# Kernel optimization log

Measured on AMD Instinct MI355X. Metric: run time of the kernel, lower is better.

## Reference

```python
import jax, jax.numpy as jnp
import numpy as np

L = 2        # num GRU layers
H = 1024     # hidden_size
V = 50257    # output_size (vocab)


def setup_inputs() -> dict:
    key = jax.random.key(0)
    ks = jax.random.split(key, 10)
    s = 1.0 / np.sqrt(H)
    return {
        "input_tok": jax.random.randint(ks[0], (1,), 0, V, dtype=jnp.int64),
        "hidden": jax.random.normal(ks[1], (L, 1, H), dtype=jnp.float32),
        "emb": jax.random.normal(ks[2], (V, H), dtype=jnp.float32),
        "W_ih": jax.random.uniform(ks[3], (L, 3 * H, H), jnp.float32, -s, s),
        "W_hh": jax.random.uniform(ks[4], (L, 3 * H, H), jnp.float32, -s, s),
        "b_ih": jax.random.uniform(ks[5], (L, 3 * H), jnp.float32, -s, s),
        "b_hh": jax.random.uniform(ks[6], (L, 3 * H), jnp.float32, -s, s),
        "W_out": jax.random.uniform(ks[7], (V, H), jnp.float32, -s, s),
        "b_out": jax.random.uniform(ks[8], (V,), jnp.float32, -s, s),
    }


def _gru_step(x, hidden, W_ih, W_hh, b_ih, b_hh):
    # x: [1, H] single-timestep input; hidden: [L, 1, H]
    # PyTorch GRU gate order: r, z, n
    new_h = []
    for l in range(L):
        h = hidden[l]                                   # [1, H]
        gi = x @ W_ih[l].T + b_ih[l]                    # [1, 3H]
        gh = h @ W_hh[l].T + b_hh[l]                    # [1, 3H]
        gi_r, gi_z, gi_n = gi[:, :H], gi[:, H:2 * H], gi[:, 2 * H:]
        gh_r, gh_z, gh_n = gh[:, :H], gh[:, H:2 * H], gh[:, 2 * H:]
        r = jax.nn.sigmoid(gi_r + gh_r)
        z = jax.nn.sigmoid(gi_z + gh_z)
        n = jnp.tanh(gi_n + r * gh_n)
        h_new = (1.0 - z) * n + z * h                   # [1, H]
        new_h.append(h_new)
        x = h_new                                       # feed next layer (eval: no dropout)
    return x, jnp.stack(new_h, axis=0)                  # [1,H], [L,1,H]


def reference(input_tok, hidden, emb, W_ih, W_hh, b_ih, b_hh, W_out, b_out):
    # embedding lookup + view(1,1,-1) -> relu
    x = jax.nn.relu(emb[input_tok[0]]).reshape(1, H)     # [1, H] (seq dim of 1 folded)
    out, hidden_new = _gru_step(x, hidden, W_ih, W_hh, b_ih, b_hh)
    logits = out @ W_out.T + b_out                       # [1, V]
    logprobs = jax.nn.log_softmax(logits, axis=1)        # LogSoftmax(dim=1)
    return logprobs, hidden_new
```

## Files before the change

### kernel.cpp

```cpp
#include <hip/hip_runtime.h>
#include <cstdint>
#include <math.h>

#define H 1024
#define V 50257
#define PBLK 2048

__device__ __forceinline__ float dot4(float4 a, float4 b) {
    return a.x * b.x + a.y * b.y + a.z * b.z + a.w * b.w;
}

__global__ __launch_bounds__(256) void gru_layer(
    const float* __restrict__ emb, const int* __restrict__ tok, int use_emb,
    const float* __restrict__ xvec,
    const float* __restrict__ hprev,
    const float* __restrict__ Wih, const float* __restrict__ Whh,
    const float* __restrict__ bih, const float* __restrict__ bhh,
    float* __restrict__ hnew_ws, float* __restrict__ hnew_out)
{
    const int i = blockIdx.x;
    const int t = threadIdx.x;

    const float* xb = use_emb ? (emb + (size_t)tok[0] * (size_t)H) : xvec;
    float4 xv = *(const float4*)(xb + 4 * t);
    if (use_emb) {
        xv.x = fmaxf(xv.x, 0.f); xv.y = fmaxf(xv.y, 0.f);
        xv.z = fmaxf(xv.z, 0.f); xv.w = fmaxf(xv.w, 0.f);
    }

    float s[6];
    {
        const float* r0 = Wih + (size_t)i * H;
        const float* r1 = Wih + (size_t)(H + i) * H;
        const float* r2 = Wih + (size_t)(2 * H + i) * H;
        const float* r3 = Whh + (size_t)i * H;
        const float* r4 = Whh + (size_t)(H + i) * H;
        const float* r5 = Whh + (size_t)(2 * H + i) * H;
        s[0] = dot4(*(const float4*)(r0 + 4 * t), xv);
        s[1] = dot4(*(const float4*)(r1 + 4 * t), xv);
        s[2] = dot4(*(const float4*)(r2 + 4 * t), xv);
        float4 hv = *(const float4*)(hprev + 4 * t);
        s[3] = dot4(*(const float4*)(r3 + 4 * t), hv);
        s[4] = dot4(*(const float4*)(r4 + 4 * t), hv);
        s[5] = dot4(*(const float4*)(r5 + 4 * t), hv);
    }

    #pragma unroll
    for (int m = 1; m < 64; m <<= 1) {
        #pragma unroll
        for (int k = 0; k < 6; ++k) s[k] += __shfl_xor(s[k], m);
    }
    __shared__ float red[4][6];
    const int wv = t >> 6, ln = t & 63;
    if (ln == 0) {
        #pragma unroll
        for (int k = 0; k < 6; ++k) red[wv][k] = s[k];
    }
    __syncthreads();
    if (t == 0) {
        float g[6];
        #pragma unroll
        for (int k = 0; k < 6; ++k)
            g[k] = red[0][k] + red[1][k] + red[2][k] + red[3][k];
        float gir = g[0] + bih[i], giz = g[1] + bih[H + i], gin = g[2] + bih[2 * H + i];
        float ghr = g[3] + bhh[i], ghz = g[4] + bhh[H + i], ghn = g[5] + bhh[2 * H + i];
        float r = 1.f / (1.f + expf(-(gir + ghr)));
        float z = 1.f / (1.f + expf(-(giz + ghz)));
        float n = tanhf(gin + r * ghn);
        float hp = hprev[i];
        float hn = (1.f - z) * n + z * hp;
        hnew_ws[i] = hn;
        hnew_out[i] = hn;
    }
}

__global__ __launch_bounds__(256) void proj_kernel(
    const float* __restrict__ h, const float* __restrict__ Wout,
    const float* __restrict__ bout, float* __restrict__ logits,
    float* __restrict__ pmax, float* __restrict__ psum)
{
    const int t = threadIdx.x;
    const int wv = t >> 6, ln = t & 63;
    const int gw = blockIdx.x * 4 + wv;
    const int nw = PBLK * 4;

    float4 hr[4];
    #pragma unroll
    for (int j = 0; j < 4; ++j) hr[j] = *(const float4*)(h + 4 * (ln + 64 * j));

    float wmax = -INFINITY, wsum = 0.f;
    for (int v = gw; v < V; v += nw) {
        const float* wrow = Wout + (size_t)v * H;
        float s = 0.f;
        #pragma unroll
        for (int j = 0; j < 4; ++j)
            s += dot4(*(const float4*)(wrow + 4 * (ln + 64 * j)), hr[j]);
        #pragma unroll
        for (int m = 1; m < 64; m <<= 1) s += __shfl_xor(s, m);
        s += bout[v];
        if (ln == 0) logits[v] = s;
        float nm = fmaxf(wmax, s);
        wsum = wsum * expf(wmax - nm) + expf(s - nm);
        wmax = nm;
    }
    __shared__ float smax[4], ssum[4];
    if (ln == 0) { smax[wv] = wmax; ssum[wv] = wsum; }
    __syncthreads();
    if (t == 0) {
        float m = fmaxf(fmaxf(smax[0], smax[1]), fmaxf(smax[2], smax[3]));
        float su = 0.f;
        #pragma unroll
        for (int w = 0; w < 4; ++w) su += ssum[w] * expf(smax[w] - m);
        pmax[blockIdx.x] = m;
        psum[blockIdx.x] = su;
    }
}

__global__ __launch_bounds__(256) void finalize_kernel(
    float* __restrict__ logits,
    const float* __restrict__ pmax, const float* __restrict__ psum)
{
    const int t = threadIdx.x;
    float m = -INFINITY, su = 0.f;
    for (int i = t; i < PBLK; i += 256) {
        float om = pmax[i], os = psum[i];
        float nm = fmaxf(m, om);
        su = su * expf(m - nm) + os * expf(om - nm);
        m = nm;
    }
    #pragma unroll
    for (int k = 1; k < 64; k <<= 1) {
        float om = __shfl_xor(m, k), os = __shfl_xor(su, k);
        float nm = fmaxf(m, om);
        su = su * expf(m - nm) + os * expf(om - nm);
        m = nm;
    }
    __shared__ float smax[4], ssum[4], slz;
    if ((t & 63) == 0) { smax[t >> 6] = m; ssum[t >> 6] = su; }
    __syncthreads();
    if (t == 0) {
        float mm = fmaxf(fmaxf(smax[0], smax[1]), fmaxf(smax[2], smax[3]));
        float ss = 0.f;
        #pragma unroll
        for (int w = 0; w < 4; ++w) ss += ssum[w] * expf(smax[w] - mm);
        slz = mm + logf(ss);
    }
    __syncthreads();
    const float lz = slz;
    for (int v = blockIdx.x * 256 + t; v < V; v += gridDim.x * 256)
        logits[v] = logits[v] - lz;
}

extern "C" void kernel_launch(void* const* d_in, const int* in_sizes, int n_in,
                              void* d_out, int out_size, void* d_ws, size_t ws_size,
                              hipStream_t stream) {
    const int*   tok    = (const int*)d_in[0];
    const float* hidden = (const float*)d_in[1];
    const float* emb    = (const float*)d_in[2];
    const float* Wih    = (const float*)d_in[3];
    const float* Whh    = (const float*)d_in[4];
    const float* bih    = (const float*)d_in[5];
    const float* bhh    = (const float*)d_in[6];
    const float* Wout   = (const float*)d_in[7];
    const float* bout   = (const float*)d_in[8];

    float* out = (float*)d_out;
    float* ws  = (float*)d_ws;
    float* pmax = ws;
    float* psum = ws + PBLK;
    float* h0 = ws + 2 * PBLK;
    float* h1 = ws + 2 * PBLK + H;

    gru_layer<<<H, 256, 0, stream>>>(emb, tok, 1, nullptr, hidden,
                                     Wih, Whh, bih, bhh, h0, out + V);
    gru_layer<<<H, 256, 0, stream>>>(nullptr, nullptr, 0, h0, hidden + H,
                                     Wih + 3 * H * H, Whh + 3 * H * H,
                                     bih + 3 * H, bhh + 3 * H, h1, out + V + H);
    proj_kernel<<<PBLK, 256, 0, stream>>>(h1, Wout, bout, out, pmax, psum);
    finalize_kernel<<<256, 256, 0, stream>>>(out, pmax, psum);
}
```

Before: 411.5 us.

## Fuse GRU layers, projection and log-softmax into one cooperative kernel

Replaces the four separate launches with one cooperative kernel of 1024 blocks that uses grid-wide syncs between the two GRU layers, the vocab projection with per-block softmax partials, and the final normalisation. The aim is to remove launch overhead and inter-kernel gaps. The projection grid drops from 2048 to 1024 blocks, so each warp handles more rows, and grid.sync adds barrier cost. A fallback to the multi-kernel path runs if the cooperative launch fails.

```diff
diff --git a/kernel.cpp b/kernel.cpp
--- a/kernel.cpp
+++ b/kernel.cpp
@@ -1,33 +1,27 @@
 #include <hip/hip_runtime.h>
+#include <hip/hip_cooperative_groups.h>
 #include <cstdint>
 #include <math.h>
 
+namespace cg = cooperative_groups;
+
 #define H 1024
 #define V 50257
-#define PBLK 2048
+#define NBLK 1024
+#define NTHR 256
 
 __device__ __forceinline__ float dot4(float4 a, float4 b) {
     return a.x * b.x + a.y * b.y + a.z * b.z + a.w * b.w;
 }
 
-__global__ __launch_bounds__(256) void gru_layer(
-    const float* __restrict__ emb, const int* __restrict__ tok, int use_emb,
-    const float* __restrict__ xvec,
+__device__ __forceinline__ void gru_elem(
+    int i, int t, float4 xv,
     const float* __restrict__ hprev,
     const float* __restrict__ Wih, const float* __restrict__ Whh,
     const float* __restrict__ bih, const float* __restrict__ bhh,
-    float* __restrict__ hnew_ws, float* __restrict__ hnew_out)
-{
-    const int i = blockIdx.x;
-    const int t = threadIdx.x;
-
-    const float* xb = use_emb ? (emb + (size_t)tok[0] * (size_t)H) : xvec;
-    float4 xv = *(const float4*)(xb + 4 * t);
-    if (use_emb) {
-        xv.x = fmaxf(xv.x, 0.f); xv.y = fmaxf(xv.y, 0.f);
-        xv.z = fmaxf(xv.z, 0.f); xv.w = fmaxf(xv.w, 0.f);
-    }
-
+    float* __restrict__ hnew_ws, float* __restrict__ hnew_out,
+    float (&red)[4][6])
+{
     float s[6];
     {
         const float* r0 = Wih + (size_t)i * H;
@@ -36,21 +30,19 @@
         const float* r3 = Whh + (size_t)i * H;
         const float* r4 = Whh + (size_t)(H + i) * H;
         const float* r5 = Whh + (size_t)(2 * H + i) * H;
+        float4 hv = *(const float4*)(hprev + 4 * t);
         s[0] = dot4(*(const float4*)(r0 + 4 * t), xv);
         s[1] = dot4(*(const float4*)(r1 + 4 * t), xv);
         s[2] = dot4(*(const float4*)(r2 + 4 * t), xv);
-        float4 hv = *(const float4*)(hprev + 4 * t);
         s[3] = dot4(*(const float4*)(r3 + 4 * t), hv);
         s[4] = dot4(*(const float4*)(r4 + 4 * t), hv);
         s[5] = dot4(*(const float4*)(r5 + 4 * t), hv);
     }
-
     #pragma unroll
     for (int m = 1; m < 64; m <<= 1) {
         #pragma unroll
         for (int k = 0; k < 6; ++k) s[k] += __shfl_xor(s[k], m);
     }
-    __shared__ float red[4][6];
     const int wv = t >> 6, ln = t & 63;
     if (ln == 0) {
         #pragma unroll
@@ -72,6 +64,130 @@
         hnew_ws[i] = hn;
         hnew_out[i] = hn;
     }
+    __syncthreads();
+}
+
+__global__ __launch_bounds__(NTHR, 4) void fused_kernel(
+    const int* __restrict__ tok, const float* __restrict__ hidden,
+    const float* __restrict__ emb,
+    const float* __restrict__ Wih, const float* __restrict__ Whh,
+    const float* __restrict__ bih, const float* __restrict__ bhh,
+    const float* __restrict__ Wout, const float* __restrict__ bout,
+    float* __restrict__ out, float* __restrict__ ws)
+{
+    cg::grid_group grid = cg::this_grid();
+    __shared__ float red[4][6];
+    __shared__ float smax[4], ssum[4], slz;
+
+    float* pmax = ws;
+    float* psum = ws + NBLK;
+    float* h0   = ws + 2 * NBLK;
+    float* h1   = h0 + H;
+
+    const int t = threadIdx.x, b = blockIdx.x;
+    const int wv = t >> 6, ln = t & 63;
+
+    {
+        const float* xb = emb + (size_t)tok[0] * (size_t)H;
+        float4 xv = *(const float4*)(xb + 4 * t);
+        xv.x = fmaxf(xv.x, 0.f); xv.y = fmaxf(xv.y, 0.f);
+        xv.z = fmaxf(xv.z, 0.f); xv.w = fmaxf(xv.w, 0.f);
+        gru_elem(b, t, xv, hidden, Wih, Whh, bih, bhh, h0, out + V, red);
+    }
+    __threadfence();
+    grid.sync();
+
+    {
+        float4 xv = *(const float4*)(h0 + 4 * t);
+        gru_elem(b, t, xv, hidden + H, Wih + 3 * H * H, Whh + 3 * H * H,
+                 bih + 3 * H, bhh + 3 * H, h1, out + V + H, red);
+    }
+    __threadfence();
+    grid.sync();
+
+    {
+        float4 hr[4];
+        #pragma unroll
+        for (int j = 0; j < 4; ++j) hr[j] = *(const float4*)(h1 + 4 * (ln + 64 * j));
+
+        const int gw = b * 4 + wv;
+        const int nw = NBLK * 4;
+        float wmax = -INFINITY, wsum = 0.f;
+        for (int v = gw; v < V; v += nw) {
+            const float* wrow = Wout + (size_t)v * H;
+            float s = 0.f;
+            #pragma unroll
+            for (int j = 0; j < 4; ++j)
+                s += dot4(*(const float4*)(wrow + 4 * (ln + 64 * j)), hr[j]);
+            #pragma unroll
+            for (int m = 1; m < 64; m <<= 1) s += __shfl_xor(s, m);
+            s += bout[v];
+            if (ln == 0) out[v] = s;
+            float nm = fmaxf(wmax, s);
+            wsum = wsum * expf(wmax - nm) + expf(s - nm);
+            wmax = nm;
+        }
+        if (ln == 0) { smax[wv] = wmax; ssum[wv] = wsum; }
+        __syncthreads();
+        if (t == 0) {
+            float m = fmaxf(fmaxf(smax[0], smax[1]), fmaxf(smax[2], smax[3]));
+            float su = 0.f;
+            #pragma unroll
+            for (int w = 0; w < 4; ++w) su += ssum[w] * expf(smax[w] - m);
+            pmax[b] = m;
+            psum[b] = su;
+        }
+    }
+    __threadfence();
+    grid.sync();
+
+    {
+        float m = -INFINITY, su = 0.f;
+        for (int i = t; i < NBLK; i += NTHR) {
+            float om = pmax[i], os = psum[i];
+            float nm = fmaxf(m, om);
+            su = su * expf(m - nm) + os * expf(om - nm);
+            m = nm;
+        }
+        #pragma unroll
+        for (int k = 1; k < 64; k <<= 1) {
+            float om = __shfl_xor(m, k), os = __shfl_xor(su, k);
+            float nm = fmaxf(m, om);
+            su = su * expf(m - nm) + os * expf(om - nm);
+            m = nm;
+        }
+        if (ln == 0) { smax[wv] = m; ssum[wv] = su; }
+        __syncthreads();
+        if (t == 0) {
+            float mm = fmaxf(fmaxf(smax[0], smax[1]), fmaxf(smax[2], smax[3]));
+            float ss = 0.f;
+            #pragma unroll
+            for (int w = 0; w < 4; ++w) ss += ssum[w] * expf(smax[w] - mm);
+            slz = mm + logf(ss);
+        }
+        __syncthreads();
+        const float lz = slz;
+        for (int v = b * NTHR + t; v < V; v += NBLK * NTHR)
+            out[v] = out[v] - lz;
+    }
+}
+
+__global__ __launch_bounds__(256) void gru_layer(
+    const float* __restrict__ emb, const int* __restrict__ tok, int use_emb,
+    const float* __restrict__ xvec, const float* __restrict__ hprev,
+    const float* __restrict__ Wih, const float* __restrict__ Whh,
+    const float* __restrict__ bih, const float* __restrict__ bhh,
+    float* __restrict__ hnew_ws, float* __restrict__ hnew_out)
+{
+    __shared__ float red[4][6];
+    const int i = blockIdx.x, t = threadIdx.x;
+    const float* xb = use_emb ? (emb + (size_t)tok[0] * (size_t)H) : xvec;
+    float4 xv = *(const float4*)(xb + 4 * t);
+    if (use_emb) {
+        xv.x = fmaxf(xv.x, 0.f); xv.y = fmaxf(xv.y, 0.f);
+        xv.z = fmaxf(xv.z, 0.f); xv.w = fmaxf(xv.w, 0.f);
+    }
+    gru_elem(i, t, xv, hprev, Wih, Whh, bih, bhh, hnew_ws, hnew_out, red);
 }
 
 __global__ __launch_bounds__(256) void proj_kernel(
@@ -79,15 +195,11 @@
     const float* __restrict__ bout, float* __restrict__ logits,
     float* __restrict__ pmax, float* __restrict__ psum)
 {
-    const int t = threadIdx.x;
-    const int wv = t >> 6, ln = t & 63;
-    const int gw = blockIdx.x * 4 + wv;
-    const int nw = PBLK * 4;
-
+    const int t = threadIdx.x, wv = t >> 6, ln = t & 63;
+    const int gw = blockIdx.x * 4 + wv, nw = NBLK * 4;
     float4 hr[4];
     #pragma unroll
     for (int j = 0; j < 4; ++j) hr[j] = *(const float4*)(h + 4 * (ln + 64 * j));
-
     float wmax = -INFINITY, wsum = 0.f;
     for (int v = gw; v < V; v += nw) {
         const float* wrow = Wout + (size_t)v * H;
@@ -122,7 +234,7 @@
 {
     const int t = threadIdx.x;
     float m = -INFINITY, su = 0.f;
-    for (int i = t; i < PBLK; i += 256) {
+    for (int i = t; i < NBLK; i += 256) {
         float om = pmax[i], os = psum[i];
         float nm = fmaxf(m, om);
         su = su * expf(m - nm) + os * expf(om - nm);
@@ -166,16 +278,24 @@
 
     float* out = (float*)d_out;
     float* ws  = (float*)d_ws;
-    float* pmax = ws;
-    float* psum = ws + PBLK;
-    float* h0 = ws + 2 * PBLK;
-    float* h1 = ws + 2 * PBLK + H;
-
-    gru_layer<<<H, 256, 0, stream>>>(emb, tok, 1, nullptr, hidden,
-                                     Wih, Whh, bih, bhh, h0, out + V);
-    gru_layer<<<H, 256, 0, stream>>>(nullptr, nullptr, 0, h0, hidden + H,
-                                     Wih + 3 * H * H, Whh + 3 * H * H,
-                                     bih + 3 * H, bhh + 3 * H, h1, out + V + H);
-    proj_kernel<<<PBLK, 256, 0, stream>>>(h1, Wout, bout, out, pmax, psum);
-    finalize_kernel<<<256, 256, 0, stream>>>(out, pmax, psum);
-}
+
+    void* args[] = {(void*)&tok, (void*)&hidden, (void*)&emb,
+                    (void*)&Wih, (void*)&Whh, (void*)&bih, (void*)&bhh,
+                    (void*)&Wout, (void*)&bout, (void*)&out, (void*)&ws};
+    hipError_t err = hipLaunchCooperativeKernel(
+        (const void*)fused_kernel, dim3(NBLK), dim3(NTHR), args, 0, stream);
+
+    if (err != hipSuccess) {
+        float* pmax = ws;
+        float* psum = ws + NBLK;
+        float* h0 = ws + 2 * NBLK;
+        float* h1 = h0 + H;
+        gru_layer<<<H, 256, 0, stream>>>(emb, tok, 1, nullptr, hidden,
+                                         Wih, Whh, bih, bhh, h0, out + V);
+        gru_layer<<<H, 256, 0, stream>>>(nullptr, nullptr, 0, h0, hidden + H,
+                                         Wih + 3 * H * H, Whh + 3 * H * H,
+                                         bih + 3 * H, bhh + 3 * H, h1, out + V + H);
+        proj_kernel<<<NBLK, 256, 0, stream>>>(h1, Wout, bout, out, pmax, psum);
+        finalize_kernel<<<256, 256, 0, stream>>>(out, pmax, psum);
+    }
+}
```

After: 939.2 us. 128% more time.
